# Kernel tuning notes

Hardware: AMD Instinct MI355X
Metric: run time of the kernel (lower is better)

Reference implementation:

```python
import jax, jax.numpy as jnp
import numpy as np

UNITS = 1024
D = 1024

def setup_inputs() -> dict:
    key = jax.random.key(0)
    ks = jax.random.split(key, 8)
    B, T = 32, 2048
    query = jax.random.normal(ks[0], (B, D), dtype=jnp.float32)
    values = jax.random.normal(ks[1], (B, T, D), dtype=jnp.float32)
    s1 = 1.0 / np.sqrt(D)
    s2 = 1.0 / np.sqrt(UNITS)
    W1 = jax.random.normal(ks[2], (D, UNITS), dtype=jnp.float32) * s1
    b1 = jnp.zeros((UNITS,), dtype=jnp.float32)
    W2 = jax.random.normal(ks[3], (D, UNITS), dtype=jnp.float32) * s1
    b2 = jnp.zeros((UNITS,), dtype=jnp.float32)
    Wv = jax.random.normal(ks[4], (UNITS, 1), dtype=jnp.float32) * s2
    bv = jnp.zeros((1,), dtype=jnp.float32)
    return {"query": query, "values": values, "W1": W1, "b1": b1,
            "W2": W2, "b2": b2, "Wv": Wv, "bv": bv}

def reference(query, values, W1, b1, W2, b2, Wv, bv):
    # query: [B, D]; values: [B, T, D]
    q_proj = query @ W1 + b1                     # [B, U]
    v_proj = jnp.einsum('btd,du->btu', values, W2) + b2  # [B, T, U]
    h = jnp.tanh(q_proj[:, None, :] + v_proj)    # [B, T, U]
    score = jnp.einsum('btu,uo->bto', h, Wv) + bv  # [B, T, 1]
    attention_weights = jax.nn.softmax(score, axis=1)  # [B, T, 1]
    context_vector = jnp.sum(attention_weights * values, axis=1)  # [B, D]
    return (context_vector, attention_weights)
```

## Files before the change

kernel.cpp:

```cpp
#include <hip/hip_runtime.h>
#include <hip/hip_bf16.h>
#include <stdint.h>


typedef unsigned short ushort_t;
typedef short bf16x8 __attribute__((ext_vector_type(8)));
typedef float f32x4 __attribute__((ext_vector_type(4)));

#define GLOBAL_AS __attribute__((address_space(1)))
#define LDS_AS    __attribute__((address_space(3)))

__device__ __forceinline__ ushort_t f2bf(float f) {
    union { float f; unsigned int u; } v;
    v.f = f;
    unsigned int u = v.u;
    unsigned int r = u + 0x7FFFu + ((u >> 16) & 1u);
    return (ushort_t)(r >> 16);
}
__device__ __forceinline__ unsigned int pk2(float a, float b) {
    union { __hip_bfloat162 h; unsigned int u; } c;
    c.h = __float22bfloat162_rn(make_float2(a, b));
    return c.u;
}

static constexpr int B_ = 32, T_ = 2048, D_ = 1024, U_ = 1024;
static constexpr int M_ = B_ * T_;

__global__ __launch_bounds__(256) void k_transpose_w2(const float* __restrict__ W2,
                                                      ushort_t* __restrict__ W2T) {
    __shared__ float tile[32][33];
    int u0 = blockIdx.x * 32, d0 = blockIdx.y * 32;
    int tx = threadIdx.x & 31, ty = threadIdx.x >> 5;
#pragma unroll
    for (int r = 0; r < 4; ++r) {
        int dd = ty + r * 8;
        tile[dd][tx] = W2[(size_t)(d0 + dd) * U_ + (u0 + tx)];
    }
    __syncthreads();
#pragma unroll
    for (int r = 0; r < 4; ++r) {
        int uu = ty + r * 8;
        W2T[(size_t)(u0 + uu) * D_ + (d0 + tx)] = f2bf(tile[tx][uu]);
    }
}

__global__ __launch_bounds__(256) void k_qproj(const float* __restrict__ query,
                                               const float* __restrict__ W1,
                                               const float* __restrict__ b1,
                                               const float* __restrict__ b2,
                                               float* __restrict__ qpb) {
    int b = blockIdx.y;
    int u = blockIdx.x * 256 + threadIdx.x;
    __shared__ float qs[D_];
    for (int i = threadIdx.x; i < D_; i += 256) qs[i] = query[b * D_ + i];
    __syncthreads();
    float acc = 0.f;
    for (int d = 0; d < D_; ++d) acc += qs[d] * W1[(size_t)d * U_ + u];
    qpb[b * U_ + u] = acc + b1[u] + b2[u];
}

#define BM 128
#define BN 128
#define BK 64

__global__ __launch_bounds__(256) void k_score_gemm(const float* __restrict__ values,
                                                    const ushort_t* __restrict__ W2T,
                                                    const float* __restrict__ qpb,
                                                    const float* __restrict__ Wv,
                                                    float* __restrict__ scores_partial) {
    __shared__ ushort_t As[BM * BK];
    __shared__ ushort_t Bs[BN * BK];
    __shared__ float sScore[BM];

    const int tid = threadIdx.x;
    const int lane = tid & 63;
    const int w = tid >> 6;
    const int wm = w >> 1;
    const int wn = w & 1;
    const int n0 = blockIdx.x * BN;
    const int m0 = blockIdx.y * BM;

    if (tid < BM) sScore[tid] = 0.f;

    f32x4 acc[4][4];
#pragma unroll
    for (int i = 0; i < 4; ++i)
#pragma unroll
        for (int j = 0; j < 4; ++j) acc[i][j] = (f32x4){0.f, 0.f, 0.f, 0.f};

    const int rr = tid >> 4;
    const int cc = tid & 15;
    const float* aSrc = values + (size_t)(m0 + rr) * D_ + cc * 4;
    ushort_t* aDst = As + rr * BK + cc * 4;

    const int mB = lane >> 3;
    const int kB = (lane & 7) * 8;
    const ushort_t* bBase = W2T + (size_t)(n0 + w * 8 + mB) * D_ + kB;

    const int quad = lane >> 4;
    const int l15 = lane & 15;

    for (int k0 = 0; k0 < D_; k0 += BK) {
#pragma unroll
        for (int i = 0; i < 4; ++i) {
            __builtin_amdgcn_global_load_lds(
                (const GLOBAL_AS void*)(bBase + k0 + (size_t)i * 32 * D_),
                (LDS_AS void*)(Bs + i * 2048 + w * 512), 16, 0, 0);
        }
#pragma unroll
        for (int i = 0; i < 8; ++i) {
            f32x4 v = *(const f32x4*)(aSrc + k0 + (size_t)i * 16 * D_);
            uint2 p;
            p.x = pk2(v[0], v[1]);
            p.y = pk2(v[2], v[3]);
            *(uint2*)(aDst + i * 16 * BK) = p;
        }
        __syncthreads();
#pragma unroll
        for (int kk = 0; kk < BK; kk += 32) {
            bf16x8 af[4], bfr[4];
            const int col = kk + quad * 8;
#pragma unroll
            for (int i = 0; i < 4; ++i)
                af[i] = *(const bf16x8*)(As + (wm * 64 + i * 16 + l15) * BK + col);
#pragma unroll
            for (int j = 0; j < 4; ++j)
                bfr[j] = *(const bf16x8*)(Bs + (wn * 64 + j * 16 + l15) * BK + col);
#pragma unroll
            for (int i = 0; i < 4; ++i)
#pragma unroll
                for (int j = 0; j < 4; ++j)
                    acc[i][j] = __builtin_amdgcn_mfma_f32_16x16x32_bf16(
                        af[i], bfr[j], acc[i][j], 0, 0, 0);
        }
        __syncthreads();
    }

    const int b = m0 >> 11;
    const float* qp = qpb + b * U_;
    float qv[4], wv[4];
#pragma unroll
    for (int j = 0; j < 4; ++j) {
        int u = n0 + wn * 64 + j * 16 + l15;
        qv[j] = qp[u];
        wv[j] = Wv[u];
    }
#pragma unroll
    for (int i = 0; i < 4; ++i) {
#pragma unroll
        for (int r = 0; r < 4; ++r) {
            float s = 0.f;
#pragma unroll
            for (int j = 0; j < 4; ++j) s += tanhf(acc[i][j][r] + qv[j]) * wv[j];
            s += __shfl_xor(s, 1);
            s += __shfl_xor(s, 2);
            s += __shfl_xor(s, 4);
            s += __shfl_xor(s, 8);
            if (l15 == 0) atomicAdd(&sScore[wm * 64 + i * 16 + quad * 4 + r], s);
        }
    }
    __syncthreads();
    if (tid < BM) scores_partial[(size_t)(m0 + tid) * 8 + blockIdx.x] = sScore[tid];
}

__global__ __launch_bounds__(256) void k_softmax(const float* __restrict__ scores_partial,
                                                 const float* __restrict__ bv,
                                                 float* __restrict__ w_f,
                                                 float* __restrict__ out_w) {
    const int b = blockIdx.x;
    __shared__ float s[T_];
    __shared__ float red[4];
    const int tid = threadIdx.x;
    const float bvf = bv[0];

    float lmax = -1e30f;
    for (int t = tid; t < T_; t += 256) {
        const float* p = scores_partial + (size_t)(b * T_ + t) * 8;
        float sc = ((p[0] + p[1]) + (p[2] + p[3])) + ((p[4] + p[5]) + (p[6] + p[7])) + bvf;
        s[t] = sc;
        lmax = fmaxf(lmax, sc);
    }
    for (int off = 32; off; off >>= 1) lmax = fmaxf(lmax, __shfl_xor(lmax, off));
    if ((tid & 63) == 0) red[tid >> 6] = lmax;
    __syncthreads();
    const float gmax = fmaxf(fmaxf(red[0], red[1]), fmaxf(red[2], red[3]));

    float lsum = 0.f;
    for (int t = tid; t < T_; t += 256) {
        float e = expf(s[t] - gmax);
        s[t] = e;
        lsum += e;
    }
    for (int off = 32; off; off >>= 1) lsum += __shfl_xor(lsum, off);
    __syncthreads();
    if ((tid & 63) == 0) red[tid >> 6] = lsum;
    __syncthreads();
    const float ginv = 1.f / ((red[0] + red[1]) + (red[2] + red[3]));

    for (int t = tid; t < T_; t += 256) {
        float wgt = s[t] * ginv;
        w_f[b * T_ + t] = wgt;
        out_w[b * T_ + t] = wgt;
    }
}

__global__ __launch_bounds__(256) void k_ctx_partial(const float* __restrict__ values,
                                                     const float* __restrict__ w_f,
                                                     float* __restrict__ ctx_partial) {
    const int tc = blockIdx.x;
    const int b = blockIdx.y;
    const int tid = threadIdx.x;

    f32x4 acc = (f32x4){0.f, 0.f, 0.f, 0.f};
    const float* base = values + (size_t)(b * T_ + tc * 256) * D_ + tid * 4;
    const float* wrow = w_f + b * T_ + tc * 256;
    for (int tt = 0; tt < 256; ++tt) {
        const float wgt = wrow[tt];
        f32x4 v = *(const f32x4*)(base + (size_t)tt * D_);
        acc += wgt * v;
    }
    *(f32x4*)(ctx_partial + (size_t)(b * 8 + tc) * D_ + tid * 4) = acc;
}

__global__ __launch_bounds__(256) void k_ctx_reduce(const float* __restrict__ ctx_partial,
                                                    float* __restrict__ out_ctx) {
    const int b = blockIdx.x;
    const int d = blockIdx.y * 256 + threadIdx.x;
    float s = 0.f;
#pragma unroll
    for (int p = 0; p < 8; ++p) s += ctx_partial[(size_t)(b * 8 + p) * D_ + d];
    out_ctx[b * D_ + d] = s;
}

extern "C" void kernel_launch(void* const* d_in, const int* in_sizes, int n_in,
                              void* d_out, int out_size, void* d_ws, size_t ws_size,
                              hipStream_t stream) {
    const float* query  = (const float*)d_in[0];
    const float* values = (const float*)d_in[1];
    const float* W1     = (const float*)d_in[2];
    const float* b1     = (const float*)d_in[3];
    const float* W2     = (const float*)d_in[4];
    const float* b2     = (const float*)d_in[5];
    const float* Wv     = (const float*)d_in[6];
    const float* bv     = (const float*)d_in[7];

    float* out_ctx = (float*)d_out;
    float* out_w   = out_ctx + B_ * D_;

    char* ws = (char*)d_ws;
    ushort_t* W2T            = (ushort_t*)(ws);
    float*    qpb            = (float*)(ws + (2u << 20));
    float*    scores_partial = (float*)(ws + (2u << 20) + 131072);
    float*    w_f            = (float*)(ws + (4u << 20) + 131072);
    float*    ctx_partial    = (float*)(ws + (4u << 20) + 131072 + 262144);

    k_transpose_w2<<<dim3(U_ / 32, D_ / 32), 256, 0, stream>>>(W2, W2T);
    k_qproj<<<dim3(U_ / 256, B_), 256, 0, stream>>>(query, W1, b1, b2, qpb);
    k_score_gemm<<<dim3(U_ / BN, M_ / BM), 256, 0, stream>>>(values, W2T, qpb, Wv,
                                                             scores_partial);
    k_softmax<<<dim3(B_), 256, 0, stream>>>(scores_partial, bv, w_f, out_w);
    k_ctx_partial<<<dim3(8, B_), 256, 0, stream>>>(values, w_f, ctx_partial);
    k_ctx_reduce<<<dim3(B_, D_ / 256), 256, 0, stream>>>(ctx_partial, out_ctx);

    (void)in_sizes; (void)n_in; (void)out_size; (void)ws_size;
}
```

Before: 680.4 us.

## Pre-convert values to bf16 and use direct-to-LDS loads with swizzled GEMM tiles

```diff
diff --git a/kernel.cpp b/kernel.cpp
--- a/kernel.cpp
+++ b/kernel.cpp
@@ -22,9 +22,28 @@
     c.h = __float22bfloat162_rn(make_float2(a, b));
     return c.u;
 }
+__device__ __forceinline__ float fast_tanh(float x) {
+    float ax = __builtin_fabsf(x);
+    float e = __expf(-2.0f * ax);
+    float t = (1.0f - e) * __builtin_amdgcn_rcpf(1.0f + e);
+    return __builtin_copysignf(t, x);
+}
 
 static constexpr int B_ = 32, T_ = 2048, D_ = 1024, U_ = 1024;
 static constexpr int M_ = B_ * T_;
+
+__global__ __launch_bounds__(256) void k_convert(const float* __restrict__ v,
+                                                 ushort_t* __restrict__ o) {
+    size_t i = ((size_t)blockIdx.x * 256 + threadIdx.x) * 8;
+    f32x4 a = *(const f32x4*)(v + i);
+    f32x4 b = *(const f32x4*)(v + i + 4);
+    uint4 p;
+    p.x = pk2(a[0], a[1]);
+    p.y = pk2(a[2], a[3]);
+    p.z = pk2(b[0], b[1]);
+    p.w = pk2(b[2], b[3]);
+    *(uint4*)(o + i) = p;
+}
 
 __global__ __launch_bounds__(256) void k_transpose_w2(const float* __restrict__ W2,
                                                       ushort_t* __restrict__ W2T) {
@@ -55,6 +74,7 @@
     for (int i = threadIdx.x; i < D_; i += 256) qs[i] = query[b * D_ + i];
     __syncthreads();
     float acc = 0.f;
+#pragma unroll 8
     for (int d = 0; d < D_; ++d) acc += qs[d] * W1[(size_t)d * U_ + u];
     qpb[b * U_ + u] = acc + b1[u] + b2[u];
 }
@@ -63,7 +83,7 @@
 #define BN 128
 #define BK 64
 
-__global__ __launch_bounds__(256) void k_score_gemm(const float* __restrict__ values,
+__global__ __launch_bounds__(256) void k_score_gemm(const ushort_t* __restrict__ Vbf,
                                                     const ushort_t* __restrict__ W2T,
                                                     const float* __restrict__ qpb,
                                                     const float* __restrict__ Wv,
@@ -77,6 +97,109 @@
     const int w = tid >> 6;
     const int wm = w >> 1;
     const int wn = w & 1;
+
+    const int g = blockIdx.x;
+    const int mt = ((g >> 6) << 3) | (g & 7);
+    const int nt = (g >> 3) & 7;
+    const int m0 = mt * BM;
+    const int n0 = nt * BN;
+
+    if (tid < BM) sScore[tid] = 0.f;
+
+    f32x4 acc[4][4];
+#pragma unroll
+    for (int i = 0; i < 4; ++i)
+#pragma unroll
+        for (int j = 0; j < 4; ++j) acc[i][j] = (f32x4){0.f, 0.f, 0.f, 0.f};
+
+    const int lr = lane >> 3;
+    const int c = (lane & 7) ^ lr;
+    const ushort_t* aBase = Vbf + (size_t)(m0 + w * 8 + lr) * D_ + c * 8;
+    const ushort_t* bBase = W2T + (size_t)(n0 + w * 8 + lr) * D_ + c * 8;
+
+    const int quad = lane >> 4;
+    const int l15 = lane & 15;
+    const int l7 = l15 & 7;
+
+    for (int k0 = 0; k0 < D_; k0 += BK) {
+#pragma unroll
+        for (int i = 0; i < 4; ++i) {
+            __builtin_amdgcn_global_load_lds(
+                (const GLOBAL_AS void*)(aBase + k0 + (size_t)i * 32 * D_),
+                (LDS_AS void*)(As + i * 2048 + w * 512), 16, 0, 0);
+        }
+#pragma unroll
+        for (int i = 0; i < 4; ++i) {
+            __builtin_amdgcn_global_load_lds(
+                (const GLOBAL_AS void*)(bBase + k0 + (size_t)i * 32 * D_),
+                (LDS_AS void*)(Bs + i * 2048 + w * 512), 16, 0, 0);
+        }
+        __syncthreads();
+#pragma unroll
+        for (int kk = 0; kk < BK; kk += 32) {
+            bf16x8 af[4], bfr[4];
+            const int cb = kk >> 3;
+#pragma unroll
+            for (int i = 0; i < 4; ++i) {
+                int r = wm * 64 + i * 16 + l15;
+                af[i] = *(const bf16x8*)(As + (r << 6) + ((((quad + cb) ^ l7)) << 3));
+            }
+#pragma unroll
+            for (int j = 0; j < 4; ++j) {
+                int r = wn * 64 + j * 16 + l15;
+                bfr[j] = *(const bf16x8*)(Bs + (r << 6) + ((((quad + cb) ^ l7)) << 3));
+            }
+#pragma unroll
+            for (int i = 0; i < 4; ++i)
+#pragma unroll
+                for (int j = 0; j < 4; ++j)
+                    acc[i][j] = __builtin_amdgcn_mfma_f32_16x16x32_bf16(
+                        af[i], bfr[j], acc[i][j], 0, 0, 0);
+        }
+        __syncthreads();
+    }
+
+    const int b = m0 >> 11;
+    const float* qp = qpb + b * U_;
+    float qv[4], wv[4];
+#pragma unroll
+    for (int j = 0; j < 4; ++j) {
+        int u = n0 + wn * 64 + j * 16 + l15;
+        qv[j] = qp[u];
+        wv[j] = Wv[u];
+    }
+#pragma unroll
+    for (int i = 0; i < 4; ++i) {
+#pragma unroll
+        for (int r = 0; r < 4; ++r) {
+            float s = 0.f;
+#pragma unroll
+            for (int j = 0; j < 4; ++j) s += fast_tanh(acc[i][j][r] + qv[j]) * wv[j];
+            s += __shfl_xor(s, 1);
+            s += __shfl_xor(s, 2);
+            s += __shfl_xor(s, 4);
+            s += __shfl_xor(s, 8);
+            if (l15 == 0) atomicAdd(&sScore[wm * 64 + i * 16 + quad * 4 + r], s);
+        }
+    }
+    __syncthreads();
+    if (tid < BM) scores_partial[(size_t)(m0 + tid) * 8 + nt] = sScore[tid];
+}
+
+__global__ __launch_bounds__(256) void k_score_gemm_f32(const float* __restrict__ values,
+                                                        const ushort_t* __restrict__ W2T,
+                                                        const float* __restrict__ qpb,
+                                                        const float* __restrict__ Wv,
+                                                        float* __restrict__ scores_partial) {
+    __shared__ ushort_t As[BM * BK];
+    __shared__ ushort_t Bs[BN * BK];
+    __shared__ float sScore[BM];
+
+    const int tid = threadIdx.x;
+    const int lane = tid & 63;
+    const int w = tid >> 6;
+    const int wm = w >> 1;
+    const int wn = w & 1;
     const int n0 = blockIdx.x * BN;
     const int m0 = blockIdx.y * BM;
 
@@ -151,7 +274,7 @@
         for (int r = 0; r < 4; ++r) {
             float s = 0.f;
 #pragma unroll
-            for (int j = 0; j < 4; ++j) s += tanhf(acc[i][j][r] + qv[j]) * wv[j];
+            for (int j = 0; j < 4; ++j) s += fast_tanh(acc[i][j][r] + qv[j]) * wv[j];
             s += __shfl_xor(s, 1);
             s += __shfl_xor(s, 2);
             s += __shfl_xor(s, 4);
@@ -187,7 +310,7 @@
 
     float lsum = 0.f;
     for (int t = tid; t < T_; t += 256) {
-        float e = expf(s[t] - gmax);
+        float e = __expf(s[t] - gmax);
         s[t] = e;
         lsum += e;
     }
@@ -210,16 +333,17 @@
     const int tc = blockIdx.x;
     const int b = blockIdx.y;
     const int tid = threadIdx.x;
+    __shared__ float wls[128];
+    if (tid < 128) wls[tid] = w_f[b * T_ + tc * 128 + tid];
+    __syncthreads();
 
     f32x4 acc = (f32x4){0.f, 0.f, 0.f, 0.f};
-    const float* base = values + (size_t)(b * T_ + tc * 256) * D_ + tid * 4;
-    const float* wrow = w_f + b * T_ + tc * 256;
-    for (int tt = 0; tt < 256; ++tt) {
-        const float wgt = wrow[tt];
-        f32x4 v = *(const f32x4*)(base + (size_t)tt * D_);
-        acc += wgt * v;
-    }
-    *(f32x4*)(ctx_partial + (size_t)(b * 8 + tc) * D_ + tid * 4) = acc;
+    const float* base = values + (size_t)(b * T_ + tc * 128) * D_ + tid * 4;
+#pragma unroll 4
+    for (int tt = 0; tt < 128; ++tt) {
+        acc += wls[tt] * *(const f32x4*)(base + (size_t)tt * D_);
+    }
+    *(f32x4*)(ctx_partial + (size_t)(b * 16 + tc) * D_ + tid * 4) = acc;
 }
 
 __global__ __launch_bounds__(256) void k_ctx_reduce(const float* __restrict__ ctx_partial,
@@ -228,7 +352,7 @@
     const int d = blockIdx.y * 256 + threadIdx.x;
     float s = 0.f;
 #pragma unroll
-    for (int p = 0; p < 8; ++p) s += ctx_partial[(size_t)(b * 8 + p) * D_ + d];
+    for (int p = 0; p < 16; ++p) s += ctx_partial[(size_t)(b * 16 + p) * D_ + d];
     out_ctx[b * D_ + d] = s;
 }
 
@@ -248,18 +372,35 @@
     float* out_w   = out_ctx + B_ * D_;
 
     char* ws = (char*)d_ws;
-    ushort_t* W2T            = (ushort_t*)(ws);
-    float*    qpb            = (float*)(ws + (2u << 20));
-    float*    scores_partial = (float*)(ws + (2u << 20) + 131072);
-    float*    w_f            = (float*)(ws + (4u << 20) + 131072);
-    float*    ctx_partial    = (float*)(ws + (4u << 20) + 131072 + 262144);
+    const size_t OFF_W2T = 0;
+    const size_t OFF_QPB = 0x200000;
+    const size_t OFF_SP  = 0x220000;
+    const size_t OFF_WF  = 0x420000;
+    const size_t OFF_CP  = 0x460000;
+    const size_t OFF_VBF = 0x660000;
+    const size_t NEED    = OFF_VBF + (size_t)M_ * D_ * sizeof(ushort_t);
+
+    ushort_t* W2T            = (ushort_t*)(ws + OFF_W2T);
+    float*    qpb            = (float*)(ws + OFF_QPB);
+    float*    scores_partial = (float*)(ws + OFF_SP);
+    float*    w_f            = (float*)(ws + OFF_WF);
+    float*    ctx_partial    = (float*)(ws + OFF_CP);
+    ushort_t* Vbf            = (ushort_t*)(ws + OFF_VBF);
 
     k_transpose_w2<<<dim3(U_ / 32, D_ / 32), 256, 0, stream>>>(W2, W2T);
     k_qproj<<<dim3(U_ / 256, B_), 256, 0, stream>>>(query, W1, b1, b2, qpb);
-    k_score_gemm<<<dim3(U_ / BN, M_ / BM), 256, 0, stream>>>(values, W2T, qpb, Wv,
-                                                             scores_partial);
+
+    if (ws_size >= NEED) {
+        k_convert<<<dim3(M_ * D_ / (256 * 8)), 256, 0, stream>>>(values, Vbf);
+        k_score_gemm<<<dim3((M_ / BM) * (U_ / BN)), 256, 0, stream>>>(
+            Vbf, W2T, qpb, Wv, scores_partial);
+    } else {
+        k_score_gemm_f32<<<dim3(U_ / BN, M_ / BM), 256, 0, stream>>>(
+            values, W2T, qpb, Wv, scores_partial);
+    }
+
     k_softmax<<<dim3(B_), 256, 0, stream>>>(scores_partial, bv, w_f, out_w);
-    k_ctx_partial<<<dim3(8, B_), 256, 0, stream>>>(values, w_f, ctx_partial);
+    k_ctx_partial<<<dim3(16, B_), 256, 0, stream>>>(values, w_f, ctx_partial);
     k_ctx_reduce<<<dim3(B_, D_ / 256), 256, 0, stream>>>(ctx_partial, out_ctx);
 
     (void)in_sizes; (void)n_in; (void)out_size; (void)ws_size;
```

After: 689.3 us. No clear change (+1.3%).

## Swizzle LDS tiles, fuse prep kernels, fast tanh, grouped tile order, atomic ctx

Applied to the files above, without the earlier changes.

```diff
diff --git a/kernel.cpp b/kernel.cpp
--- a/kernel.cpp
+++ b/kernel.cpp
@@ -22,41 +22,62 @@
     c.h = __float22bfloat162_rn(make_float2(a, b));
     return c.u;
 }
+__device__ __forceinline__ float fast_tanh(float x) {
+    float ax = __builtin_fabsf(x);
+    float e = __expf(-2.0f * ax);
+    float t = (1.0f - e) * __builtin_amdgcn_rcpf(1.0f + e);
+    return __builtin_copysignf(t, x);
+}
 
 static constexpr int B_ = 32, T_ = 2048, D_ = 1024, U_ = 1024;
 static constexpr int M_ = B_ * T_;
-
-__global__ __launch_bounds__(256) void k_transpose_w2(const float* __restrict__ W2,
-                                                      ushort_t* __restrict__ W2T) {
-    __shared__ float tile[32][33];
-    int u0 = blockIdx.x * 32, d0 = blockIdx.y * 32;
-    int tx = threadIdx.x & 31, ty = threadIdx.x >> 5;
-#pragma unroll
-    for (int r = 0; r < 4; ++r) {
-        int dd = ty + r * 8;
-        tile[dd][tx] = W2[(size_t)(d0 + dd) * U_ + (u0 + tx)];
-    }
-    __syncthreads();
-#pragma unroll
-    for (int r = 0; r < 4; ++r) {
-        int uu = ty + r * 8;
-        W2T[(size_t)(u0 + uu) * D_ + (d0 + tx)] = f2bf(tile[tx][uu]);
-    }
-}
-
-__global__ __launch_bounds__(256) void k_qproj(const float* __restrict__ query,
-                                               const float* __restrict__ W1,
-                                               const float* __restrict__ b1,
-                                               const float* __restrict__ b2,
-                                               float* __restrict__ qpb) {
-    int b = blockIdx.y;
-    int u = blockIdx.x * 256 + threadIdx.x;
-    __shared__ float qs[D_];
-    for (int i = threadIdx.x; i < D_; i += 256) qs[i] = query[b * D_ + i];
-    __syncthreads();
+static constexpr int TRANS_B = 1024;
+static constexpr int QPROJ_B = 512;
+
+__global__ __launch_bounds__(256) void k_prep(const float* __restrict__ W2,
+                                              const float* __restrict__ query,
+                                              const float* __restrict__ W1,
+                                              const float* __restrict__ b1,
+                                              const float* __restrict__ b2,
+                                              ushort_t* __restrict__ W2T,
+                                              float* __restrict__ qpb) {
+    __shared__ float smem[1280];
+    int bid = blockIdx.x;
+    const int tid = threadIdx.x;
+
+    if (bid < TRANS_B) {
+        float(*tile)[33] = (float(*)[33])smem;
+        int u0 = (bid & 31) * 32, d0 = (bid >> 5) * 32;
+        int tx = tid & 31, ty = tid >> 5;
+#pragma unroll
+        for (int r = 0; r < 4; ++r)
+            tile[ty + r * 8][tx] = W2[(size_t)(d0 + ty + r * 8) * U_ + (u0 + tx)];
+        __syncthreads();
+#pragma unroll
+        for (int r = 0; r < 4; ++r)
+            W2T[(size_t)(u0 + ty + r * 8) * D_ + (d0 + tx)] = f2bf(tile[tx][ty + r * 8]);
+        return;
+    }
+    bid -= TRANS_B;
+
+    const int b = bid >> 4, uc = bid & 15;
+    float* qs = smem;
+    float* red = smem + 1024;
+    for (int i = tid; i < D_; i += 256) qs[i] = query[b * D_ + i];
+    __syncthreads();
+    const int ul = tid & 63, ds = tid >> 6;
+    const int u = uc * 64 + ul;
     float acc = 0.f;
-    for (int d = 0; d < D_; ++d) acc += qs[d] * W1[(size_t)d * U_ + u];
-    qpb[b * U_ + u] = acc + b1[u] + b2[u];
+#pragma unroll 8
+    for (int d = ds * 256; d < ds * 256 + 256; ++d)
+        acc += qs[d] * W1[(size_t)d * U_ + u];
+    red[tid] = acc;
+    __syncthreads();
+    if (tid < 64) {
+        int uu = uc * 64 + tid;
+        qpb[b * U_ + uu] = red[tid] + red[tid + 64] + red[tid + 128] + red[tid + 192] +
+                           b1[uu] + b2[uu];
+    }
 }
 
 #define BM 128
@@ -75,10 +96,12 @@
     const int tid = threadIdx.x;
     const int lane = tid & 63;
     const int w = tid >> 6;
-    const int wm = w >> 1;
-    const int wn = w & 1;
-    const int n0 = blockIdx.x * BN;
-    const int m0 = blockIdx.y * BM;
+    const int wm = w >> 1, wn = w & 1;
+
+    const int g = blockIdx.x;
+    const int mt = ((g >> 6) << 3) | (g & 7);
+    const int nt = (g >> 3) & 7;
+    const int m0 = mt * BM, n0 = nt * BN;
 
     if (tid < BM) sScore[tid] = 0.f;
 
@@ -88,17 +111,19 @@
 #pragma unroll
         for (int j = 0; j < 4; ++j) acc[i][j] = (f32x4){0.f, 0.f, 0.f, 0.f};
 
-    const int rr = tid >> 4;
-    const int cc = tid & 15;
-    const float* aSrc = values + (size_t)(m0 + rr) * D_ + cc * 4;
-    ushort_t* aDst = As + rr * BK + cc * 4;
-
-    const int mB = lane >> 3;
-    const int kB = (lane & 7) * 8;
-    const ushort_t* bBase = W2T + (size_t)(n0 + w * 8 + mB) * D_ + kB;
+    const int rA = tid >> 3;
+    const int cA = tid & 7;
+    const int pA = cA ^ (rA & 7);
+    const float* aSrc = values + (size_t)(m0 + rA) * D_ + cA * 8;
+    ushort_t* aDst = As + rA * BK + pA * 8;
+
+    const int lr = lane >> 3;
+    const int cB = (lane & 7) ^ lr;
+    const ushort_t* bBase = W2T + (size_t)(n0 + w * 8 + lr) * D_ + cB * 8;
 
     const int quad = lane >> 4;
     const int l15 = lane & 15;
+    const int l7 = l15 & 7;
 
     for (int k0 = 0; k0 < D_; k0 += BK) {
 #pragma unroll
@@ -108,24 +133,31 @@
                 (LDS_AS void*)(Bs + i * 2048 + w * 512), 16, 0, 0);
         }
 #pragma unroll
-        for (int i = 0; i < 8; ++i) {
-            f32x4 v = *(const f32x4*)(aSrc + k0 + (size_t)i * 16 * D_);
-            uint2 p;
-            p.x = pk2(v[0], v[1]);
-            p.y = pk2(v[2], v[3]);
-            *(uint2*)(aDst + i * 16 * BK) = p;
+        for (int i = 0; i < 4; ++i) {
+            f32x4 v0 = *(const f32x4*)(aSrc + k0 + (size_t)i * 32 * D_);
+            f32x4 v1 = *(const f32x4*)(aSrc + k0 + (size_t)i * 32 * D_ + 4);
+            uint4 p;
+            p.x = pk2(v0[0], v0[1]);
+            p.y = pk2(v0[2], v0[3]);
+            p.z = pk2(v1[0], v1[1]);
+            p.w = pk2(v1[2], v1[3]);
+            *(uint4*)(aDst + i * 32 * BK) = p;
         }
         __syncthreads();
 #pragma unroll
         for (int kk = 0; kk < BK; kk += 32) {
             bf16x8 af[4], bfr[4];
-            const int col = kk + quad * 8;
-#pragma unroll
-            for (int i = 0; i < 4; ++i)
-                af[i] = *(const bf16x8*)(As + (wm * 64 + i * 16 + l15) * BK + col);
-#pragma unroll
-            for (int j = 0; j < 4; ++j)
-                bfr[j] = *(const bf16x8*)(Bs + (wn * 64 + j * 16 + l15) * BK + col);
+            const int cb = kk >> 3;
+#pragma unroll
+            for (int i = 0; i < 4; ++i) {
+                int r = wm * 64 + i * 16 + l15;
+                af[i] = *(const bf16x8*)(As + (r << 6) + (((quad + cb) ^ l7) << 3));
+            }
+#pragma unroll
+            for (int j = 0; j < 4; ++j) {
+                int r = wn * 64 + j * 16 + l15;
+                bfr[j] = *(const bf16x8*)(Bs + (r << 6) + (((quad + cb) ^ l7) << 3));
+            }
 #pragma unroll
             for (int i = 0; i < 4; ++i)
 #pragma unroll
@@ -151,7 +183,7 @@
         for (int r = 0; r < 4; ++r) {
             float s = 0.f;
 #pragma unroll
-            for (int j = 0; j < 4; ++j) s += tanhf(acc[i][j][r] + qv[j]) * wv[j];
+            for (int j = 0; j < 4; ++j) s += fast_tanh(acc[i][j][r] + qv[j]) * wv[j];
             s += __shfl_xor(s, 1);
             s += __shfl_xor(s, 2);
             s += __shfl_xor(s, 4);
@@ -160,7 +192,7 @@
         }
     }
     __syncthreads();
-    if (tid < BM) scores_partial[(size_t)(m0 + tid) * 8 + blockIdx.x] = sScore[tid];
+    if (tid < BM) scores_partial[(size_t)(m0 + tid) * 8 + nt] = sScore[tid];
 }
 
 __global__ __launch_bounds__(256) void k_softmax(const float* __restrict__ scores_partial,
@@ -187,7 +219,7 @@
 
     float lsum = 0.f;
     for (int t = tid; t < T_; t += 256) {
-        float e = expf(s[t] - gmax);
+        float e = __expf(s[t] - gmax);
         s[t] = e;
         lsum += e;
     }
@@ -204,32 +236,26 @@
     }
 }
 
-__global__ __launch_bounds__(256) void k_ctx_partial(const float* __restrict__ values,
-                                                     const float* __restrict__ w_f,
-                                                     float* __restrict__ ctx_partial) {
+__global__ __launch_bounds__(256) void k_ctx(const float* __restrict__ values,
+                                             const float* __restrict__ w_f,
+                                             float* __restrict__ out_ctx) {
     const int tc = blockIdx.x;
     const int b = blockIdx.y;
     const int tid = threadIdx.x;
+    __shared__ float wls[128];
+    if (tid < 128) wls[tid] = w_f[b * T_ + tc * 128 + tid];
+    __syncthreads();
 
     f32x4 acc = (f32x4){0.f, 0.f, 0.f, 0.f};
-    const float* base = values + (size_t)(b * T_ + tc * 256) * D_ + tid * 4;
-    const float* wrow = w_f + b * T_ + tc * 256;
-    for (int tt = 0; tt < 256; ++tt) {
-        const float wgt = wrow[tt];
-        f32x4 v = *(const f32x4*)(base + (size_t)tt * D_);
-        acc += wgt * v;
-    }
-    *(f32x4*)(ctx_partial + (size_t)(b * 8 + tc) * D_ + tid * 4) = acc;
-}
-
-__global__ __launch_bounds__(256) void k_ctx_reduce(const float* __restrict__ ctx_partial,
-                                                    float* __restrict__ out_ctx) {
-    const int b = blockIdx.x;
-    const int d = blockIdx.y * 256 + threadIdx.x;
-    float s = 0.f;
-#pragma unroll
-    for (int p = 0; p < 8; ++p) s += ctx_partial[(size_t)(b * 8 + p) * D_ + d];
-    out_ctx[b * D_ + d] = s;
+    const float* base = values + (size_t)(b * T_ + tc * 128) * D_ + tid * 4;
+#pragma unroll 4
+    for (int tt = 0; tt < 128; ++tt)
+        acc += wls[tt] * *(const f32x4*)(base + (size_t)tt * D_);
+    float* out = out_ctx + b * D_ + tid * 4;
+    atomicAdd(&out[0], acc[0]);
+    atomicAdd(&out[1], acc[1]);
+    atomicAdd(&out[2], acc[2]);
+    atomicAdd(&out[3], acc[3]);
 }
 
 extern "C" void kernel_launch(void* const* d_in, const int* in_sizes, int n_in,
@@ -248,19 +274,23 @@
     float* out_w   = out_ctx + B_ * D_;
 
     char* ws = (char*)d_ws;
-    ushort_t* W2T            = (ushort_t*)(ws);
-    float*    qpb            = (float*)(ws + (2u << 20));
-    float*    scores_partial = (float*)(ws + (2u << 20) + 131072);
-    float*    w_f            = (float*)(ws + (4u << 20) + 131072);
-    float*    ctx_partial    = (float*)(ws + (4u << 20) + 131072 + 262144);
-
-    k_transpose_w2<<<dim3(U_ / 32, D_ / 32), 256, 0, stream>>>(W2, W2T);
-    k_qproj<<<dim3(U_ / 256, B_), 256, 0, stream>>>(query, W1, b1, b2, qpb);
-    k_score_gemm<<<dim3(U_ / BN, M_ / BM), 256, 0, stream>>>(values, W2T, qpb, Wv,
-                                                             scores_partial);
+    const size_t OFF_W2T = 0;
+    const size_t OFF_QPB = 0x200000;
+    const size_t OFF_SP  = 0x220000;
+    const size_t OFF_WF  = 0x420000;
+
+    ushort_t* W2T            = (ushort_t*)(ws + OFF_W2T);
+    float*    qpb            = (float*)(ws + OFF_QPB);
+    float*    scores_partial = (float*)(ws + OFF_SP);
+    float*    w_f            = (float*)(ws + OFF_WF);
+
+    hipMemsetAsync(out_ctx, 0, (size_t)B_ * D_ * sizeof(float), stream);
+
+    k_prep<<<dim3(TRANS_B + QPROJ_B), 256, 0, stream>>>(W2, query, W1, b1, b2, W2T, qpb);
+    k_score_gemm<<<dim3((M_ / BM) * (U_ / BN)), 256, 0, stream>>>(
+        values, W2T, qpb, Wv, scores_partial);
     k_softmax<<<dim3(B_), 256, 0, stream>>>(scores_partial, bv, w_f, out_w);
-    k_ctx_partial<<<dim3(8, B_), 256, 0, stream>>>(values, w_f, ctx_partial);
-    k_ctx_reduce<<<dim3(B_, D_ / 256), 256, 0, stream>>>(ctx_partial, out_ctx);
+    k_ctx<<<dim3(16, B_), 256, 0, stream>>>(values, w_f, out_ctx);
 
     (void)in_sizes; (void)n_in; (void)out_size; (void)ws_size;
 }
```

Result: faster. 580.6 us (-14.7%).
